# Kernel optimization log

Measured on AMD Instinct MI355X. Metric: run time of the kernel, lower is better.

The kernel has to match this reference:

```python
import jax, jax.numpy as jnp
import numpy as np

N, E, R, K1, F = 50000, 400000, 1000, 1000, 128
DEPTH, HEADS = 1, 2

def _l2norm(x, axis):
    n = jnp.sqrt(jnp.maximum(jnp.sum(x * x, axis=axis, keepdims=True), 1e-12))
    return x / n

def _segment_softmax(logits, seg, num_segments):
    m = jax.ops.segment_max(logits, seg, num_segments=num_segments)
    e = jnp.exp(logits - m[seg])
    s = jax.ops.segment_sum(e, seg, num_segments=num_segments)
    return e / s[seg]

def setup_inputs() -> dict:
    rng = np.random.RandomState(0)
    # adjacency: nodes 0..K1-1 have exactly one edge (long-tail), rest random rows
    rows = np.concatenate([np.arange(K1), rng.randint(K1, N, size=E - K1)])
    cols = rng.randint(0, N, size=E)
    order = np.lexsort((cols, rows))
    adj = np.stack([rows, cols], axis=1)[order].astype(np.int32)  # [E,2] sorted by row
    self_nodes_idx = np.arange(K1, dtype=np.int32)
    neights_node_idxs = adj[:K1, 1].astype(np.int32)  # neighbor of each degree-1 node
    sparse_indices = np.stack([np.arange(E), rng.randint(0, R, size=E)], axis=1).astype(np.int32)
    sparse_val = (rng.rand(E).astype(np.float32) * 0.5 + 0.5)
    key = jax.random.key(0)
    k = jax.random.split(key, 5)
    return {
        'features': jax.random.normal(k[0], (N, F), jnp.float32),
        'rel_emb': jax.random.normal(k[1], (R, F), jnp.float32),
        'sparse_val': jnp.asarray(sparse_val),
        'attn_kernels': jax.random.normal(k[2], (DEPTH, HEADS, F), jnp.float32) * (1.0 / np.sqrt(F)),
        'proxy': jax.random.normal(k[3], (64, F * (DEPTH + 1)), jnp.float32) * 0.1,
        'gate_kernel': jax.random.normal(k[4], (F * (DEPTH + 1), F * (DEPTH + 1)), jnp.float32) * (1.0 / np.sqrt(F * (DEPTH + 1))),
        'adj_indices': jnp.asarray(adj),
        'sparse_indices': jnp.asarray(sparse_indices),
        'self_nodes_idx': jnp.asarray(self_nodes_idx),
        'neights_node_idxs': jnp.asarray(neights_node_idxs),
    }

def reference(features, rel_emb, sparse_val, attn_kernels, proxy, gate_kernel,
              adj_indices, sparse_indices, self_nodes_idx, neights_node_idxs):
    row = adj_indices[:, 0]
    col = adj_indices[:, 1]
    feats = features  # activation is linear (None)
    outputs = [feats]
    for l in range(DEPTH):
        # per-triple relation embedding: sparse (E,R) @ rel_emb -> (E,F)
        rels_sum = jax.ops.segment_sum(sparse_val[:, None] * rel_emb[sparse_indices[:, 1]],
                                       sparse_indices[:, 0], num_segments=E)
        rels_norm = _l2norm(rels_sum, axis=1)  # l2 normalize rows
        neighs = feats[col]  # [E,F] gather
        # Householder reflection of neighbor features by relation direction
        neighs = neighs - 2.0 * jnp.sum(neighs * rels_norm, axis=1, keepdims=True) * rels_norm
        head_feats = []
        for head in range(HEADS):
            att_logits = rels_sum @ attn_kernels[l, head]  # [E]
            att = _segment_softmax(att_logits, row, N)  # sparse softmax per destination node
            nf = jax.ops.segment_sum(neighs * att[:, None], row, num_segments=N)  # [N,F]
            if head == 1:
                # long-tail fix: degree-1 nodes copy their single neighbor's aggregated feature
                nf = nf.at[self_nodes_idx].set(nf[neights_node_idxs])
            head_feats.append(nf)
        feats = jnp.mean(jnp.stack(head_feats, axis=0), axis=0)
        outputs.append(feats)
    out = jnp.concatenate(outputs, axis=-1)  # [N, F*(DEPTH+1)]
    proxy_att = jax.nn.softmax(_l2norm(out, axis=-1) @ _l2norm(proxy, axis=-1).T, axis=-1)  # [N,64]
    proxy_feature = out - proxy_att @ proxy
    gate = jax.nn.sigmoid(proxy_feature @ gate_kernel)
    return gate * out + (1.0 - gate) * proxy_feature
```

## Files before the change

kernel.cpp:

```cpp
#include <hip/hip_runtime.h>
#include <math.h>

constexpr int N  = 50000;
constexpr int E  = 400000;
constexpr int R  = 1000;
constexpr int K1 = 1000;
constexpr int F  = 128;
constexpr int OUTC = 256;
constexpr int P  = 64;

typedef _Float16 f16x8 __attribute__((ext_vector_type(8)));
typedef _Float16 f16x4 __attribute__((ext_vector_type(4)));
typedef _Float16 f16x2 __attribute__((ext_vector_type(2)));
typedef float f32x4 __attribute__((ext_vector_type(4)));

#if __has_builtin(__builtin_amdgcn_fdot2)
#define FDOT2(a, b, c) __builtin_amdgcn_fdot2((a), (b), (c), false)
#else
#define FDOT2(a, b, c) fmaf((float)(a)[0], (float)(b)[0], fmaf((float)(a)[1], (float)(b)[1], (c)))
#endif

__device__ inline float waveReduceSum(float v) {
#pragma unroll
    for (int m = 32; m >= 1; m >>= 1) v += __shfl_xor(v, m, 64);
    return v;
}

constexpr int B_FEATSH = 3125;
constexpr int B_REL    = 250;
constexpr int B_SEG    = 1563;
constexpr int B_PSC    = 16;
constexpr int B_PGF    = 64;

__global__ __launch_bounds__(256) void prep_a(
        const float* __restrict__ feats, const float* __restrict__ rel_emb,
        const float* __restrict__ attn,  const float* __restrict__ proxy,
        const float* __restrict__ G,     const int* __restrict__ adj,
        _Float16* __restrict__ featsH,   _Float16* __restrict__ relnormH,
        float* __restrict__ dotr, int* __restrict__ nstart, int* __restrict__ nend,
        float* __restrict__ pscale, float* __restrict__ PGf) {
    int b = blockIdx.x, tid = threadIdx.x;
    if (b < B_FEATSH) {
        int idx = b * 256 + tid;
        float4 x0 = ((const float4*)feats)[2 * idx];
        float4 x1 = ((const float4*)feats)[2 * idx + 1];
        f16x8 h;
        h[0] = (_Float16)x0.x; h[1] = (_Float16)x0.y;
        h[2] = (_Float16)x0.z; h[3] = (_Float16)x0.w;
        h[4] = (_Float16)x1.x; h[5] = (_Float16)x1.y;
        h[6] = (_Float16)x1.z; h[7] = (_Float16)x1.w;
        ((f16x8*)featsH)[idx] = h;
    } else if (b < B_FEATSH + B_REL) {
        int r = (b - B_FEATSH) * 4 + (tid >> 6);
        int lane = tid & 63;
        float2 v  = ((const float2*)(rel_emb + (size_t)r * F))[lane];
        float2 a0 = ((const float2*)attn)[lane];
        float2 a1 = ((const float2*)attn)[64 + lane];
        float ss = waveReduceSum(v.x * v.x + v.y * v.y);
        float d0 = waveReduceSum(v.x * a0.x + v.y * a0.y);
        float d1 = waveReduceSum(v.x * a1.x + v.y * a1.y);
        float sc = rsqrtf(fmaxf(ss, 1e-12f));
        f16x2 h; h[0] = (_Float16)(v.x * sc); h[1] = (_Float16)(v.y * sc);
        ((f16x2*)(relnormH + (size_t)r * F))[lane] = h;
        if (lane == 0) { dotr[2 * r] = d0; dotr[2 * r + 1] = d1; }
    } else if (b < B_FEATSH + B_REL + B_SEG) {
        int e = (b - B_FEATSH - B_REL) * 256 + tid;
        if (e < E) {
            int lane = tid & 63;
            int row = ((const int2*)adj)[e].x;
            int prev = __shfl_up(row, 1, 64);
            if (lane == 0) prev = (e > 0) ? ((const int2*)adj)[e - 1].x : -1;
            int nxt = __shfl_down(row, 1, 64);
            if (lane == 63 && e + 1 < E) nxt = ((const int2*)adj)[e + 1].x;
            if (prev != row) {
                nstart[row] = e;
                for (int rr = prev + 1; rr < row; ++rr) { nstart[rr] = e; nend[rr] = e; }
            }
            if (e == E - 1) {
                nend[row] = E;
                for (int rr = row + 1; rr < N; ++rr) { nstart[rr] = E; nend[rr] = E; }
            } else if (nxt != row) {
                nend[row] = e + 1;
            }
        }
    } else if (b < B_FEATSH + B_REL + B_SEG + B_PSC) {
        int j = (b - B_FEATSH - B_REL - B_SEG) * 4 + (tid >> 6);
        int lane = tid & 63;
        float4 p = ((const float4*)(proxy + (size_t)j * OUTC))[lane];
        float ss = waveReduceSum(p.x * p.x + p.y * p.y + p.z * p.z + p.w * p.w);
        if (lane == 0) pscale[j] = rsqrtf(fmaxf(ss, 1e-12f));
    } else {
        int p = b - (B_FEATSH + B_REL + B_SEG + B_PSC);
        int c = tid;
        float s = 0.f;
        for (int k = 0; k < OUTC; ++k)
            s = fmaf(proxy[(size_t)p * OUTC + k], G[(size_t)k * OUTC + c], s);
        PGf[(size_t)p * OUTC + c] = s;
    }
}

constexpr int NB_NODE = N / 4;
constexpr int NB_FRAG = 56;

__global__ __launch_bounds__(256) void node_frag(
        const _Float16* __restrict__ featsH,
        const _Float16* __restrict__ relnormH,
        const float* __restrict__ dotr,
        const int* __restrict__ adj,
        const int* __restrict__ sidx,
        const float* __restrict__ val,
        const int* __restrict__ nstart,
        const int* __restrict__ nend,
        const float* __restrict__ G,
        const float* __restrict__ proxy,
        const float* __restrict__ pscale,
        const float* __restrict__ PGf,
        _Float16* __restrict__ nf0,
        _Float16* __restrict__ nf1,
        f16x8* __restrict__ Gh, f16x8* __restrict__ pnH,
        f16x8* __restrict__ pxH, f16x8* __restrict__ pgH) {
    if (blockIdx.x >= NB_NODE) {
        int u = (blockIdx.x - NB_NODE) * 4 + (threadIdx.x >> 6);
        int L = threadIdx.x & 63;
        int q = L >> 4, m = L & 15;
        f16x8 h;
        if (u < 128) {
            int kk = u >> 4, cg = u & 15;
            int n = cg * 16 + m;
#pragma unroll
            for (int j = 0; j < 8; ++j)
                h[j] = (_Float16)G[(size_t)(kk * 32 + q * 8 + j) * OUTC + n];
            Gh[(size_t)u * 64 + L] = h;
        } else if (u < 160) {
            int idx = u - 128;
            int kk = idx >> 2, w = idx & 3;
            int n = w * 16 + m;
            float sc = pscale[n];
#pragma unroll
            for (int j = 0; j < 8; ++j)
                h[j] = (_Float16)(proxy[(size_t)n * OUTC + kk * 32 + q * 8 + j] * sc);
            pnH[(size_t)idx * 64 + L] = h;
        } else if (u < 192) {
            int idx = u - 160;
            int kk = idx >> 4, cg = idx & 15;
            int n = cg * 16 + m;
#pragma unroll
            for (int j = 0; j < 8; ++j)
                h[j] = (_Float16)proxy[(size_t)(kk * 32 + q * 8 + j) * OUTC + n];
            pxH[(size_t)idx * 64 + L] = h;
        } else {
            int idx = u - 192;
            int kk = idx >> 4, cg = idx & 15;
            int n = cg * 16 + m;
#pragma unroll
            for (int j = 0; j < 8; ++j)
                h[j] = (_Float16)(-PGf[(size_t)(kk * 32 + q * 8 + j) * OUTC + n]);
            pgH[(size_t)idx * 64 + L] = h;
        }
        return;
    }
    int n = blockIdx.x * 4 + (threadIdx.x >> 6);
    int lane = threadIdx.x & 63;
    int g = lane >> 4, gl = lane & 15;
    int start = nstart[n], end = nend[n];
    const int2* adj2 = (const int2*)adj;
    const int2* sx2  = (const int2*)sidx;
    float A0[8], A1[8];
#pragma unroll
    for (int j = 0; j < 8; ++j) { A0[j] = 0.f; A1[j] = 0.f; }
    float s0 = 0.f, s1 = 0.f;
    for (int e = start + g; e < end; e += 8) {
        int eB = e + 4;
        bool hasB = (eB < end);
        int eBc = hasB ? eB : e;
        int colA = adj2[e].y,   colB = adj2[eBc].y;
        int relA = sx2[e].y,    relB = sx2[eBc].y;
        float vA = val[e],      vB = val[eBc];
        float2 drA = ((const float2*)dotr)[relA];
        float2 drB = ((const float2*)dotr)[relB];
        float wA0 = __expf(vA * drA.x), wA1 = __expf(vA * drA.y);
        float wB0 = hasB ? __expf(vB * drB.x) : 0.f;
        float wB1 = hasB ? __expf(vB * drB.y) : 0.f;
        s0 += wA0 + wB0; s1 += wA1 + wB1;
        f16x8 fAv = ((const f16x8*)(featsH   + (size_t)colA * F))[gl];
        f16x8 rAv = ((const f16x8*)(relnormH + (size_t)relA * F))[gl];
        f16x8 fBv = ((const f16x8*)(featsH   + (size_t)colB * F))[gl];
        f16x8 rBv = ((const f16x8*)(relnormH + (size_t)relB * F))[gl];
        const f16x2* fA2 = (const f16x2*)&fAv;
        const f16x2* rA2 = (const f16x2*)&rAv;
        const f16x2* fB2 = (const f16x2*)&fBv;
        const f16x2* rB2 = (const f16x2*)&rBv;
        float pdA = 0.f, pdB = 0.f;
#pragma unroll
        for (int j = 0; j < 4; ++j) {
            pdA = FDOT2(fA2[j], rA2[j], pdA);
            pdB = FDOT2(fB2[j], rB2[j], pdB);
        }
        pdA += __shfl_xor(pdA, 1, 64); pdB += __shfl_xor(pdB, 1, 64);
        pdA += __shfl_xor(pdA, 2, 64); pdB += __shfl_xor(pdB, 2, 64);
        pdA += __shfl_xor(pdA, 4, 64); pdB += __shfl_xor(pdB, 4, 64);
        pdA += __shfl_xor(pdA, 8, 64); pdB += __shfl_xor(pdB, 8, 64);
        _Float16 tAh = (_Float16)(2.f * pdA), tBh = (_Float16)(2.f * pdB);
        f16x2 tA2; tA2[0] = tAh; tA2[1] = tAh;
        f16x2 tB2; tB2[0] = tBh; tB2[1] = tBh;
#pragma unroll
        for (int j = 0; j < 4; ++j) {
            f16x2 rxA = fA2[j] - tA2 * rA2[j];
            f16x2 rxB = fB2[j] - tB2 * rB2[j];
            float x0 = (float)rxA[0], x1 = (float)rxA[1];
            float y0 = (float)rxB[0], y1 = (float)rxB[1];
            A0[2*j]   = fmaf(wA0, x0, A0[2*j]);   A0[2*j]   = fmaf(wB0, y0, A0[2*j]);
            A0[2*j+1] = fmaf(wA0, x1, A0[2*j+1]); A0[2*j+1] = fmaf(wB0, y1, A0[2*j+1]);
            A1[2*j]   = fmaf(wA1, x0, A1[2*j]);   A1[2*j]   = fmaf(wB1, y0, A1[2*j]);
            A1[2*j+1] = fmaf(wA1, x1, A1[2*j+1]); A1[2*j+1] = fmaf(wB1, y1, A1[2*j+1]);
        }
    }
#pragma unroll
    for (int j = 0; j < 8; ++j) {
        A0[j] += __shfl_xor(A0[j], 16, 64); A0[j] += __shfl_xor(A0[j], 32, 64);
        A1[j] += __shfl_xor(A1[j], 16, 64); A1[j] += __shfl_xor(A1[j], 32, 64);
    }
    s0 += __shfl_xor(s0, 16, 64); s0 += __shfl_xor(s0, 32, 64);
    s1 += __shfl_xor(s1, 16, 64); s1 += __shfl_xor(s1, 32, 64);
    float i0 = (s0 > 0.f) ? 1.f / s0 : 0.f;
    float i1 = (s1 > 0.f) ? 1.f / s1 : 0.f;
    if (g == 0) {
        f16x8 h0, h1;
#pragma unroll
        for (int j = 0; j < 8; ++j) {
            h0[j] = (_Float16)(A0[j] * i0);
            h1[j] = (_Float16)(A1[j] * i1);
        }
        ((f16x8*)(nf0 + (size_t)n * F))[gl] = h0;
        ((f16x8*)(nf1 + (size_t)n * F))[gl] = h1;
    }
}

__global__ __launch_bounds__(256, 8) void proxy_gate(
        const _Float16* __restrict__ featsH,
        const _Float16* __restrict__ nf0,
        const _Float16* __restrict__ nf1,
        const int* __restrict__ neigh,
        const f16x8* __restrict__ pnH,
        const f16x8* __restrict__ pxH,
        const f16x8* __restrict__ Gh,
        const f16x8* __restrict__ pgH,
        float* __restrict__ out) {
    constexpr int LDA = 68;
    __shared__ __align__(16) f16x8 outH[8 * 64];
    __shared__ __align__(16) float attL[16 * LDA];
    __shared__ float scaleL[16];
    int tid = threadIdx.x;
    int w = tid >> 6, lane = tid & 63;
    int quad = lane >> 4, m = lane & 15;
    size_t row0 = (size_t)blockIdx.x * 16;

    {
        int bm = tid >> 4, gl = tid & 15;
        int n = (int)row0 + bm;
        float ss;
        f16x8 h1, h2;
        if (n < N) {
            ss = 0.f;
            h1 = ((const f16x8*)(featsH + (size_t)n * F))[gl];
#pragma unroll
            for (int j = 0; j < 8; ++j) { float x = (float)h1[j]; ss += x * x; }
            int sel = (n < K1) ? neigh[n] : n;
            f16x8 a  = ((const f16x8*)(nf0 + (size_t)n   * F))[gl];
            f16x8 b2 = ((const f16x8*)(nf1 + (size_t)sel * F))[gl];
#pragma unroll
            for (int j = 0; j < 8; ++j) {
                float v = 0.5f * ((float)a[j] + (float)b2[j]);
                h2[j] = (_Float16)v;
                ss += v * v;
            }
        } else {
#pragma unroll
            for (int j = 0; j < 8; ++j) { h1[j] = (_Float16)0.f; h2[j] = (_Float16)0.f; }
            ss = 1.f;
        }
        outH[((gl >> 2)) * 64 + (gl & 3) * 16 + bm] = h1;
        outH[(4 + (gl >> 2)) * 64 + (gl & 3) * 16 + bm] = h2;
        ss += __shfl_xor(ss, 1, 64); ss += __shfl_xor(ss, 2, 64);
        ss += __shfl_xor(ss, 4, 64); ss += __shfl_xor(ss, 8, 64);
        if (gl == 0) scaleL[bm] = rsqrtf(fmaxf(ss, 1e-12f));
    }
    __syncthreads();

    f32x4 lacc = (f32x4){0,0,0,0};
    f32x4 zacc[4];
#pragma unroll
    for (int c = 0; c < 4; ++c) zacc[c] = (f32x4){0,0,0,0};
#pragma unroll
    for (int kk = 0; kk < 8; ++kk) {
        f16x8 pb  = pnH[(size_t)(kk * 4 + w) * 64 + lane];
        f16x8 gb0 = Gh[(size_t)(kk * 16 + w +  0) * 64 + lane];
        f16x8 gb1 = Gh[(size_t)(kk * 16 + w +  4) * 64 + lane];
        f16x8 gb2 = Gh[(size_t)(kk * 16 + w +  8) * 64 + lane];
        f16x8 gb3 = Gh[(size_t)(kk * 16 + w + 12) * 64 + lane];
        f16x8 a = outH[kk * 64 + lane];
        lacc    = __builtin_amdgcn_mfma_f32_16x16x32_f16(a, pb,  lacc,    0, 0, 0);
        zacc[0] = __builtin_amdgcn_mfma_f32_16x16x32_f16(a, gb0, zacc[0], 0, 0, 0);
        zacc[1] = __builtin_amdgcn_mfma_f32_16x16x32_f16(a, gb1, zacc[1], 0, 0, 0);
        zacc[2] = __builtin_amdgcn_mfma_f32_16x16x32_f16(a, gb2, zacc[2], 0, 0, 0);
        zacc[3] = __builtin_amdgcn_mfma_f32_16x16x32_f16(a, gb3, zacc[3], 0, 0, 0);
    }
#pragma unroll
    for (int i = 0; i < 4; ++i) {
        int r = quad * 4 + i;
        attL[r * LDA + w * 16 + m] = lacc[i] * scaleL[r];
    }
    __syncthreads();

#pragma unroll
    for (int i = 0; i < 4; ++i) {
        int r = 4 * w + i;
        float e = __expf(attL[r * LDA + lane]);
        float s = waveReduceSum(e);
        attL[r * LDA + lane] = e / s;
    }
    __syncthreads();

    f32x4 qacc[4];
#pragma unroll
    for (int c = 0; c < 4; ++c) qacc[c] = (f32x4){0,0,0,0};
#pragma unroll
    for (int kk = 0; kk < 2; ++kk) {
        f16x8 a;
        {
            const float4* ap = (const float4*)&attL[m * LDA + kk * 32 + quad * 8];
            float4 x = ap[0], y = ap[1];
            a[0]=(_Float16)x.x; a[1]=(_Float16)x.y; a[2]=(_Float16)x.z; a[3]=(_Float16)x.w;
            a[4]=(_Float16)y.x; a[5]=(_Float16)y.y; a[6]=(_Float16)y.z; a[7]=(_Float16)y.w;
        }
#pragma unroll
        for (int cgi = 0; cgi < 4; ++cgi) {
            int cg = w + 4 * cgi;
            f16x8 bx = pxH[(size_t)(kk * 16 + cg) * 64 + lane];
            f16x8 bg = pgH[(size_t)(kk * 16 + cg) * 64 + lane];
            qacc[cgi] = __builtin_amdgcn_mfma_f32_16x16x32_f16(a, bx, qacc[cgi], 0, 0, 0);
            zacc[cgi] = __builtin_amdgcn_mfma_f32_16x16x32_f16(a, bg, zacc[cgi], 0, 0, 0);
        }
    }

    const _Float16* outHs = (const _Float16*)outH;
    if ((int)row0 < N) {
#pragma unroll
        for (int cgi = 0; cgi < 4; ++cgi) {
            int cg = w + 4 * cgi;
            int c = cg * 16 + m;
            int kkc = cg >> 1;
            int qc = ((cg & 1) << 1) | (m >> 3);
            int j = m & 7;
#pragma unroll
            for (int i = 0; i < 4; ++i) {
                int r15 = quad * 4 + i;
                float ov = (float)outHs[(((kkc) * 64 + qc * 16 + r15) << 3) + j];
                float gate = 1.f / (1.f + __expf(-zacc[cgi][i]));
                size_t n = row0 + r15;
                out[n * OUTC + c] = ov - (1.f - gate) * qacc[cgi][i];
            }
        }
    }
}

extern "C" void kernel_launch(void* const* d_in, const int* in_sizes, int n_in,
                              void* d_out, int out_size, void* d_ws, size_t ws_size,
                              hipStream_t stream) {
    const float* features   = (const float*)d_in[0];
    const float* rel_emb    = (const float*)d_in[1];
    const float* sparse_val = (const float*)d_in[2];
    const float* attn       = (const float*)d_in[3];
    const float* proxy      = (const float*)d_in[4];
    const float* gateK      = (const float*)d_in[5];
    const int*   adj        = (const int*)d_in[6];
    const int*   sidx       = (const int*)d_in[7];
    const int*   neigh      = (const int*)d_in[9];
    float* out = (float*)d_out;

    char* ws = (char*)d_ws;
    size_t off = 0;
    auto alloc = [&](size_t bytes) -> void* {
        void* p = ws + off;
        off += (bytes + 255) & ~(size_t)255;
        return p;
    };
    _Float16* relnormH = (_Float16*)alloc((size_t)R * F * 2);
    float*    dotr     = (float*)alloc((size_t)R * 2 * 4);
    float*    pscale   = (float*)alloc((size_t)P * 4);
    float*    PGf      = (float*)alloc((size_t)P * OUTC * 4);
    f16x8*    Gh       = (f16x8*)alloc((size_t)128 * 64 * 16);
    f16x8*    pnH      = (f16x8*)alloc((size_t)32 * 64 * 16);
    f16x8*    pxH      = (f16x8*)alloc((size_t)32 * 64 * 16);
    f16x8*    pgH      = (f16x8*)alloc((size_t)32 * 64 * 16);
    _Float16* featsH   = (_Float16*)alloc((size_t)N * F * 2);
    int*      nstart   = (int*)alloc((size_t)N * 4);
    int*      nend     = (int*)alloc((size_t)N * 4);
    _Float16* nf0      = (_Float16*)alloc((size_t)N * F * 2);
    _Float16* nf1      = (_Float16*)alloc((size_t)N * F * 2);

    prep_a<<<B_FEATSH + B_REL + B_SEG + B_PSC + B_PGF, 256, 0, stream>>>(
        features, rel_emb, attn, proxy, gateK, adj,
        featsH, relnormH, dotr, nstart, nend, pscale, PGf);
    node_frag<<<NB_NODE + NB_FRAG, 256, 0, stream>>>(
        featsH, relnormH, dotr, adj, sidx, sparse_val, nstart, nend,
        gateK, proxy, pscale, PGf,
        nf0, nf1, Gh, pnH, pxH, pgH);
    proxy_gate<<<N / 16, 256, 0, stream>>>(
        featsH, nf0, nf1, neigh, pnH, pxH, Gh, pgH, out);
}
```

Before: 175.1 us.

## Process 32 rows per proxy_gate block with 8 waves sharing gate-kernel fragments

Doubles the proxy_gate tile from 16 to 32 rows per block and uses 512 threads (8 waves). Each wave now computes two row tiles against two column groups, so every gate-kernel and proxy B-fragment it loads is reused across both row tiles. This halves per-row global loads of the weight fragments and halves the block count. The cost is more shared memory and registers per block, a larger launch, and a bounds change from (256,8) to (512,6) that may lower occupancy.

```diff
diff --git a/kernel.cpp b/kernel.cpp
--- a/kernel.cpp
+++ b/kernel.cpp
@@ -236,7 +236,7 @@
     }
 }
 
-__global__ __launch_bounds__(256, 8) void proxy_gate(
+__global__ __launch_bounds__(512, 6) void proxy_gate(
         const _Float16* __restrict__ featsH,
         const _Float16* __restrict__ nf0,
         const _Float16* __restrict__ nf1,
@@ -247,13 +247,13 @@
         const f16x8* __restrict__ pgH,
         float* __restrict__ out) {
     constexpr int LDA = 68;
-    __shared__ __align__(16) f16x8 outH[8 * 64];
-    __shared__ __align__(16) float attL[16 * LDA];
-    __shared__ float scaleL[16];
+    __shared__ __align__(16) f16x8 outH[16 * 64];
+    __shared__ __align__(16) float attL[32 * LDA];
+    __shared__ float scaleL[32];
     int tid = threadIdx.x;
     int w = tid >> 6, lane = tid & 63;
     int quad = lane >> 4, m = lane & 15;
-    size_t row0 = (size_t)blockIdx.x * 16;
+    size_t row0 = (size_t)blockIdx.x * 32;
 
     {
         int bm = tid >> 4, gl = tid & 15;
@@ -279,36 +279,41 @@
             for (int j = 0; j < 8; ++j) { h1[j] = (_Float16)0.f; h2[j] = (_Float16)0.f; }
             ss = 1.f;
         }
-        outH[((gl >> 2)) * 64 + (gl & 3) * 16 + bm] = h1;
-        outH[(4 + (gl >> 2)) * 64 + (gl & 3) * 16 + bm] = h2;
+        int t = bm >> 4, r16 = bm & 15;
+        outH[(t * 8 +     (gl >> 2)) * 64 + (gl & 3) * 16 + r16] = h1;
+        outH[(t * 8 + 4 + (gl >> 2)) * 64 + (gl & 3) * 16 + r16] = h2;
         ss += __shfl_xor(ss, 1, 64); ss += __shfl_xor(ss, 2, 64);
         ss += __shfl_xor(ss, 4, 64); ss += __shfl_xor(ss, 8, 64);
         if (gl == 0) scaleL[bm] = rsqrtf(fmaxf(ss, 1e-12f));
     }
     __syncthreads();
 
+    int tl = w >> 2;
+    int pg = w & 3;
     f32x4 lacc = (f32x4){0,0,0,0};
-    f32x4 zacc[4];
-#pragma unroll
-    for (int c = 0; c < 4; ++c) zacc[c] = (f32x4){0,0,0,0};
+    f32x4 zacc[2][2];
+#pragma unroll
+    for (int t = 0; t < 2; ++t)
+#pragma unroll
+        for (int c = 0; c < 2; ++c) zacc[t][c] = (f32x4){0,0,0,0};
 #pragma unroll
     for (int kk = 0; kk < 8; ++kk) {
-        f16x8 pb  = pnH[(size_t)(kk * 4 + w) * 64 + lane];
-        f16x8 gb0 = Gh[(size_t)(kk * 16 + w +  0) * 64 + lane];
-        f16x8 gb1 = Gh[(size_t)(kk * 16 + w +  4) * 64 + lane];
-        f16x8 gb2 = Gh[(size_t)(kk * 16 + w +  8) * 64 + lane];
-        f16x8 gb3 = Gh[(size_t)(kk * 16 + w + 12) * 64 + lane];
-        f16x8 a = outH[kk * 64 + lane];
-        lacc    = __builtin_amdgcn_mfma_f32_16x16x32_f16(a, pb,  lacc,    0, 0, 0);
-        zacc[0] = __builtin_amdgcn_mfma_f32_16x16x32_f16(a, gb0, zacc[0], 0, 0, 0);
-        zacc[1] = __builtin_amdgcn_mfma_f32_16x16x32_f16(a, gb1, zacc[1], 0, 0, 0);
-        zacc[2] = __builtin_amdgcn_mfma_f32_16x16x32_f16(a, gb2, zacc[2], 0, 0, 0);
-        zacc[3] = __builtin_amdgcn_mfma_f32_16x16x32_f16(a, gb3, zacc[3], 0, 0, 0);
+        f16x8 pb  = pnH[(size_t)(kk * 4 + pg) * 64 + lane];
+        f16x8 gb0 = Gh[(size_t)(kk * 16 + w)     * 64 + lane];
+        f16x8 gb1 = Gh[(size_t)(kk * 16 + w + 8) * 64 + lane];
+        f16x8 a0 = outH[(0 * 8 + kk) * 64 + lane];
+        f16x8 a1 = outH[(1 * 8 + kk) * 64 + lane];
+        f16x8 at = tl ? a1 : a0;
+        lacc       = __builtin_amdgcn_mfma_f32_16x16x32_f16(at, pb,  lacc,       0, 0, 0);
+        zacc[0][0] = __builtin_amdgcn_mfma_f32_16x16x32_f16(a0, gb0, zacc[0][0], 0, 0, 0);
+        zacc[0][1] = __builtin_amdgcn_mfma_f32_16x16x32_f16(a0, gb1, zacc[0][1], 0, 0, 0);
+        zacc[1][0] = __builtin_amdgcn_mfma_f32_16x16x32_f16(a1, gb0, zacc[1][0], 0, 0, 0);
+        zacc[1][1] = __builtin_amdgcn_mfma_f32_16x16x32_f16(a1, gb1, zacc[1][1], 0, 0, 0);
     }
 #pragma unroll
     for (int i = 0; i < 4; ++i) {
-        int r = quad * 4 + i;
-        attL[r * LDA + w * 16 + m] = lacc[i] * scaleL[r];
+        int r = tl * 16 + quad * 4 + i;
+        attL[r * LDA + pg * 16 + m] = lacc[i] * scaleL[r];
     }
     __syncthreads();
 
@@ -321,33 +326,41 @@
     }
     __syncthreads();
 
-    f32x4 qacc[4];
-#pragma unroll
-    for (int c = 0; c < 4; ++c) qacc[c] = (f32x4){0,0,0,0};
+    f32x4 qacc[2][2];
+#pragma unroll
+    for (int t = 0; t < 2; ++t)
+#pragma unroll
+        for (int c = 0; c < 2; ++c) qacc[t][c] = (f32x4){0,0,0,0};
 #pragma unroll
     for (int kk = 0; kk < 2; ++kk) {
-        f16x8 a;
-        {
-            const float4* ap = (const float4*)&attL[m * LDA + kk * 32 + quad * 8];
+        f16x8 a[2];
+#pragma unroll
+        for (int t = 0; t < 2; ++t) {
+            const float4* ap = (const float4*)&attL[(t * 16 + m) * LDA + kk * 32 + quad * 8];
             float4 x = ap[0], y = ap[1];
-            a[0]=(_Float16)x.x; a[1]=(_Float16)x.y; a[2]=(_Float16)x.z; a[3]=(_Float16)x.w;
-            a[4]=(_Float16)y.x; a[5]=(_Float16)y.y; a[6]=(_Float16)y.z; a[7]=(_Float16)y.w;
-        }
-#pragma unroll
-        for (int cgi = 0; cgi < 4; ++cgi) {
-            int cg = w + 4 * cgi;
+            a[t][0]=(_Float16)x.x; a[t][1]=(_Float16)x.y; a[t][2]=(_Float16)x.z; a[t][3]=(_Float16)x.w;
+            a[t][4]=(_Float16)y.x; a[t][5]=(_Float16)y.y; a[t][6]=(_Float16)y.z; a[t][7]=(_Float16)y.w;
+        }
+#pragma unroll
+        for (int cgi = 0; cgi < 2; ++cgi) {
+            int cg = w + 8 * cgi;
             f16x8 bx = pxH[(size_t)(kk * 16 + cg) * 64 + lane];
             f16x8 bg = pgH[(size_t)(kk * 16 + cg) * 64 + lane];
-            qacc[cgi] = __builtin_amdgcn_mfma_f32_16x16x32_f16(a, bx, qacc[cgi], 0, 0, 0);
-            zacc[cgi] = __builtin_amdgcn_mfma_f32_16x16x32_f16(a, bg, zacc[cgi], 0, 0, 0);
+#pragma unroll
+            for (int t = 0; t < 2; ++t) {
+                qacc[t][cgi] = __builtin_amdgcn_mfma_f32_16x16x32_f16(a[t], bx, qacc[t][cgi], 0, 0, 0);
+                zacc[t][cgi] = __builtin_amdgcn_mfma_f32_16x16x32_f16(a[t], bg, zacc[t][cgi], 0, 0, 0);
+            }
         }
     }
 
     const _Float16* outHs = (const _Float16*)outH;
-    if ((int)row0 < N) {
-#pragma unroll
-        for (int cgi = 0; cgi < 4; ++cgi) {
-            int cg = w + 4 * cgi;
+#pragma unroll
+    for (int t = 0; t < 2; ++t) {
+        if ((int)row0 + t * 16 >= N) continue;
+#pragma unroll
+        for (int cgi = 0; cgi < 2; ++cgi) {
+            int cg = w + 8 * cgi;
             int c = cg * 16 + m;
             int kkc = cg >> 1;
             int qc = ((cg & 1) << 1) | (m >> 3);
@@ -355,10 +368,10 @@
 #pragma unroll
             for (int i = 0; i < 4; ++i) {
                 int r15 = quad * 4 + i;
-                float ov = (float)outHs[(((kkc) * 64 + qc * 16 + r15) << 3) + j];
-                float gate = 1.f / (1.f + __expf(-zacc[cgi][i]));
-                size_t n = row0 + r15;
-                out[n * OUTC + c] = ov - (1.f - gate) * qacc[cgi][i];
+                float ov = (float)outHs[(((t * 8 + kkc) * 64 + qc * 16 + r15) << 3) + j];
+                float gate = 1.f / (1.f + __expf(-zacc[t][cgi][i]));
+                size_t n = row0 + t * 16 + r15;
+                out[n * OUTC + c] = ov - (1.f - gate) * qacc[t][cgi][i];
             }
         }
     }
@@ -406,6 +419,6 @@
         featsH, relnormH, dotr, adj, sidx, sparse_val, nstart, nend,
         gateK, proxy, pscale, PGf,
         nf0, nf1, Gh, pnH, pxH, pgH);
-    proxy_gate<<<N / 16, 256, 0, stream>>>(
+    proxy_gate<<<(N + 31) / 32, 512, 0, stream>>>(
         featsH, nf0, nf1, neigh, pnH, pxH, Gh, pgH, out);
 }
```

After: 172.8 us. About the same (-1.3%).
